# Performance work log

Measured on AMD Instinct MI355X. Metric: run time of the kernel, lower is better.

## Reference

```python
import jax, jax.numpy as jnp
import numpy as np

ALPHA = 0.34          # Ewald splitting parameter (init kwarg alpha)
MAX_HKL = 12          # init kwarg max_hkl
TWO_PI = 2.0 * np.pi


def setup_inputs() -> dict:
    key = jax.random.key(0)
    k1, k2 = jax.random.split(key)
    N = 4096
    L = 40.0  # cubic box edge (Angstrom)
    coords = jax.random.uniform(k1, (N, 3), dtype=jnp.float32) * L
    q = jax.random.normal(k2, (N,), dtype=jnp.float32)
    q = q - jnp.mean(q)  # neutral cell (k=0 term is excluded)
    box = jnp.eye(3, dtype=jnp.float32) * L
    return {"coords": coords, "box": box, "q": q}


def _ewald_recip_energy(coords, box, q):
    """Reciprocal-space Ewald sum over |h|,|k|,|l| <= MAX_HKL (rank=0 PME fallback).

    pot_i = (4*pi/V) * sum_{k!=0} exp(-|k|^2/(4 a^2))/|k|^2 * Re[S(k) exp(-i k.r_i)]
    E     = 0.5 * sum_i q_i * pot_i
    """
    K = MAX_HKL
    vol = jnp.abs(jnp.linalg.det(box))
    recip = TWO_PI * jnp.linalg.inv(box).T  # rows = reciprocal lattice vectors (3,3)
    h = jnp.arange(-K, K + 1)
    hh, kk, ll = jnp.meshgrid(h, h, h, indexing="ij")
    hkl = jnp.stack([hh.ravel(), kk.ravel(), ll.ravel()], axis=-1).astype(jnp.float32)  # (Nk,3)
    kvecs = hkl @ recip                      # (Nk,3)
    k2 = jnp.sum(kvecs * kvecs, axis=-1)     # (Nk,)
    nonzero = k2 > 0.0                       # mask out k = 0 (static shape, jit-safe)
    k2_safe = jnp.where(nonzero, k2, 1.0)
    inv_4a2 = 1.0 / (4.0 * ALPHA * ALPHA)
    fac = jnp.where(nonzero, jnp.exp(-k2_safe * inv_4a2) / k2_safe, 0.0)  # (Nk,)
    phases = coords @ kvecs.T                # (N, Nk)
    c = jnp.cos(phases)
    s = jnp.sin(phases)
    Sre = q @ c                              # (Nk,) Re S(k)
    Sim = q @ s                              # (Nk,) Im S(k)
    pref = (4.0 * np.pi) / vol
    # Re[S(k) e^{-i k.r_i}] = Sre*cos + Sim*sin
    pot = pref * (c @ (fac * Sre) + s @ (fac * Sim))  # (N,)
    return 0.5 * jnp.sum(q * pot)


def reference(coords, box, q):
    return _ewald_recip_energy(coords, box, q)
```

## Files before the change

### kernel.cpp

```cpp
#include <hip/hip_runtime.h>
#include <math.h>

namespace {
constexpr int   KMAX   = 12;
constexpr int   NLINE  = 313;
constexpr int   NGROUP = NLINE * 5;
constexpr int   NKV    = NGROUP * 5;
constexpr int   NSLICE = 8;
constexpr int   S2_BLOCKS = (NKV + 255) / 256;
constexpr float ALPHA_  = 0.34f;
constexpr float TWO_PI_ = 6.283185307179586f;
}

__device__ __forceinline__ void cofactors(const float* __restrict__ box,
                                          float C[3][3], float* det) {
  const float b00 = box[0], b01 = box[1], b02 = box[2];
  const float b10 = box[3], b11 = box[4], b12 = box[5];
  const float b20 = box[6], b21 = box[7], b22 = box[8];
  C[0][0] =  (b11 * b22 - b12 * b21);
  C[0][1] = -(b10 * b22 - b12 * b20);
  C[0][2] =  (b10 * b21 - b11 * b20);
  C[1][0] = -(b01 * b22 - b02 * b21);
  C[1][1] =  (b00 * b22 - b02 * b20);
  C[1][2] = -(b00 * b21 - b01 * b20);
  C[2][0] =  (b01 * b12 - b02 * b11);
  C[2][1] = -(b00 * b12 - b02 * b10);
  C[2][2] =  (b00 * b11 - b01 * b10);
  *det = b00 * C[0][0] + b01 * C[0][1] + b02 * C[0][2];
}

__device__ __forceinline__ void line_hk(int L, int* h, int* k) {
  if (L < 300)      { *h = L / 25 + 1; *k = L % 25 - 12; }
  else if (L < 312) { *h = 0;          *k = L - 299;     }
  else              { *h = 0;          *k = 0;           }
}

__global__ __launch_bounds__(256) void make_frac(
    const float* __restrict__ coords, const float* __restrict__ box,
    const float* __restrict__ q, int N, float4* __restrict__ frac,
    float* __restrict__ out)
{
  const int i = blockIdx.x * 256 + threadIdx.x;
  if (i == 0) out[0] = 0.0f;
  if (i >= N) return;
  float C[3][3], det;
  cofactors(box, C, &det);
  const float invdet = 1.0f / det;
  const float x = coords[3 * i + 0];
  const float y = coords[3 * i + 1];
  const float z = coords[3 * i + 2];
  float4 f;
  f.x = (x * C[0][0] + y * C[0][1] + z * C[0][2]) * invdet;
  f.y = (x * C[1][0] + y * C[1][1] + z * C[1][2]) * invdet;
  float c = (x * C[2][0] + y * C[2][1] + z * C[2][2]) * invdet;
  f.z = c - floorf(c);
  f.w = q[i];
  frac[i] = f;
}

__global__ __launch_bounds__(256, 8) void ewald_g5(
    const float4* __restrict__ frac, int N, float* __restrict__ partial)
{
  const int lane = threadIdx.x & 63;
  const int g    = blockIdx.x * 4 + (threadIdx.x >> 6);
  const int gc   = (g < NGROUP) ? g : (NGROUP - 1);

  int h, k; line_hk(gc / 5, &h, &k);
  const float hf  = (float)h;
  const float kf  = (float)k;
  const float l0f = (float)(-KMAX + 5 * (gc % 5));

  const int slice = blockIdx.y;
  const int sp    = (N + NSLICE - 1) / NSLICE;
  const int s_beg = slice * sp;
  const int s_end = min(s_beg + sp, N);

  float Sre[5] = {0.f, 0.f, 0.f, 0.f, 0.f};
  float Sim[5] = {0.f, 0.f, 0.f, 0.f, 0.f};

  for (int i = s_beg + lane; i < s_end; i += 64) {
    const float4 p = frac[i];
    float t = fmaf(hf, p.x, fmaf(kf, p.y, l0f * p.z));
    float tf;
    asm("v_fract_f32 %0, %1" : "=v"(tf) : "v"(t));
    float s0, c0, sr, cr;
    asm("v_sin_f32 %0, %1" : "=v"(s0) : "v"(tf));
    asm("v_cos_f32 %0, %1" : "=v"(c0) : "v"(tf));
    asm("v_sin_f32 %0, %1" : "=v"(sr) : "v"(p.z));
    asm("v_cos_f32 %0, %1" : "=v"(cr) : "v"(p.z));
    float Pre = p.w * c0, Pim = p.w * s0;
    Sre[0] += Pre; Sim[0] += Pim;
#pragma unroll
    for (int u = 1; u < 5; ++u) {
      const float nre = fmaf(Pre, cr, -(Pim * sr));
      const float nim = fmaf(Pre, sr,  (Pim * cr));
      Pre = nre; Pim = nim;
      Sre[u] += Pre; Sim[u] += Pim;
    }
  }

#pragma unroll
  for (int off = 32; off > 0; off >>= 1) {
#pragma unroll
    for (int u = 0; u < 5; ++u) {
      Sre[u] += __shfl_down(Sre[u], off);
      Sim[u] += __shfl_down(Sim[u], off);
    }
  }
  if (g < NGROUP && lane == 0) {
    float* dst = partial + (size_t)(g * NSLICE + slice) * 10;
#pragma unroll
    for (int u = 0; u < 5; ++u) {
      dst[2 * u + 0] = Sre[u];
      dst[2 * u + 1] = Sim[u];
    }
  }
}

__global__ __launch_bounds__(256) void stage2(
    const float* __restrict__ partial, const float* __restrict__ box,
    float* __restrict__ out)
{
  __shared__ float red[256];
  const int idx = blockIdx.x * 256 + threadIdx.x;
  float e = 0.f;
  if (idx < NKV) {
    const int g = idx / 5, u = idx % 5;
    const int L = g / 5, sub = g % 5;
    int h, k; line_hk(L, &h, &k);
    const int l = -KMAX + 5 * sub + u;
    if (!(h == 0 && k == 0 && l <= 0)) {
      float re = 0.f, im = 0.f;
      for (int s = 0; s < NSLICE; ++s) {
        const float* p = partial + (size_t)(g * NSLICE + s) * 10 + 2 * u;
        re += p[0]; im += p[1];
      }
      float C[3][3], det;
      cofactors(box, C, &det);
      const float invdet = 1.0f / det;
      const float hf = (float)h, kf = (float)k, lf = (float)l;
      const float kx = (hf * C[0][0] + kf * C[1][0] + lf * C[2][0]) * invdet;
      const float ky = (hf * C[0][1] + kf * C[1][1] + lf * C[2][1]) * invdet;
      const float kz = (hf * C[0][2] + kf * C[1][2] + lf * C[2][2]) * invdet;
      const float k2 = TWO_PI_ * TWO_PI_ * (kx * kx + ky * ky + kz * kz);
      const float fac = __expf(-k2 / (4.0f * ALPHA_ * ALPHA_)) / k2;
      e = fac * fmaf(re, re, im * im);
    }
  }
  red[threadIdx.x] = e;
  __syncthreads();
  for (int s = 128; s > 0; s >>= 1) {
    if (threadIdx.x < s) red[threadIdx.x] += red[threadIdx.x + s];
    __syncthreads();
  }
  if (threadIdx.x == 0) {
    float C[3][3], det;
    cofactors(box, C, &det);
    const float scale = (4.0f * 3.14159265358979323846f) / fabsf(det);
    atomicAdd(out, scale * red[0]);
  }
}

extern "C" void kernel_launch(void* const* d_in, const int* in_sizes, int n_in,
                              void* d_out, int out_size, void* d_ws, size_t ws_size,
                              hipStream_t stream) {
  const float* coords = (const float*)d_in[0];
  const float* box    = (const float*)d_in[1];
  const float* q      = (const float*)d_in[2];
  float* out = (float*)d_out;
  const int N = in_sizes[2];

  float4* frac    = (float4*)d_ws;
  float*  partial = (float*)((char*)d_ws + (128 << 10));

  hipLaunchKernelGGL(make_frac, dim3((N + 255) / 256), dim3(256), 0, stream,
                     coords, box, q, N, frac, out);
  const dim3 grid((NGROUP + 3) / 4, NSLICE);
  hipLaunchKernelGGL(ewald_g5, grid, dim3(256), 0, stream, frac, N, partial);
  hipLaunchKernelGGL(stage2, dim3(S2_BLOCKS), dim3(256), 0, stream,
                     partial, box, out);
}
```

Before: 24.96 us.

## Factor structure factors into hk-line by l GEMM on fp16 MFMA

Splits exp(i(h a + k b + l c)) into an (h,k) phase table and an l phase table, built as fp16 matrices over atoms. The per-k-vector sum then becomes a complex GEMM run with 16x16x32 fp16 MFMA instructions, and the per-atom sin/cos and complex rotation loops go away. The cost is writing about 5.7 MB of fp16 intermediates to workspace, plus reduced precision from fp16 operands. It also hardcodes KDIM=4096, which ties the kernel to N<=4096.

```diff
diff --git a/kernel.cpp b/kernel.cpp
--- a/kernel.cpp
+++ b/kernel.cpp
@@ -4,12 +4,20 @@
 namespace {
 constexpr int   KMAX   = 12;
 constexpr int   NLINE  = 313;
-constexpr int   NGROUP = NLINE * 5;
-constexpr int   NKV    = NGROUP * 5;
-constexpr int   NSLICE = 8;
+constexpr int   NL25   = 25;
+constexpr int   NKV    = NLINE * NL25;
+constexpr int   KDIM   = 4096;
+constexpr int   MROWS  = 640;
+constexpr int   NCOLS  = 64;
+constexpr int   NKS    = 8;
+constexpr int   KCHUNK = KDIM / NKS;
 constexpr int   S2_BLOCKS = (NKV + 255) / 256;
 constexpr float ALPHA_  = 0.34f;
 constexpr float TWO_PI_ = 6.283185307179586f;
+
+typedef __attribute__((ext_vector_type(4))) short    short4v;
+typedef __attribute__((ext_vector_type(8))) _Float16 half8;
+typedef __attribute__((ext_vector_type(4))) float    f32x4;
 }
 
 __device__ __forceinline__ void cofactors(const float* __restrict__ box,
@@ -35,105 +43,116 @@
   else              { *h = 0;          *k = 0;           }
 }
 
-__global__ __launch_bounds__(256) void make_frac(
+__global__ __launch_bounds__(256) void build_ab(
     const float* __restrict__ coords, const float* __restrict__ box,
-    const float* __restrict__ q, int N, float4* __restrict__ frac,
+    const float* __restrict__ q, int N,
+    _Float16* __restrict__ A2, _Float16* __restrict__ Bt,
     float* __restrict__ out)
 {
-  const int i = blockIdx.x * 256 + threadIdx.x;
-  if (i == 0) out[0] = 0.0f;
-  if (i >= N) return;
+  const int id = blockIdx.x * 256 + threadIdx.x;
+  if (id == 0) out[0] = 0.0f;
+
   float C[3][3], det;
   cofactors(box, C, &det);
   const float invdet = 1.0f / det;
-  const float x = coords[3 * i + 0];
-  const float y = coords[3 * i + 1];
-  const float z = coords[3 * i + 2];
-  float4 f;
-  f.x = (x * C[0][0] + y * C[0][1] + z * C[0][2]) * invdet;
-  f.y = (x * C[1][0] + y * C[1][1] + z * C[1][2]) * invdet;
-  float c = (x * C[2][0] + y * C[2][1] + z * C[2][2]) * invdet;
-  f.z = c - floorf(c);
-  f.w = q[i];
-  frac[i] = f;
-}
-
-__global__ __launch_bounds__(256, 8) void ewald_g5(
-    const float4* __restrict__ frac, int N, float* __restrict__ partial)
+
+  if (id < 320 * KDIM) {
+    const int Ls = id >> 12;
+    const int i  = id & (KDIM - 1);
+    float pr = 0.f, pi_ = 0.f;
+    if (Ls < NLINE && i < N) {
+      int h, k; line_hk(Ls, &h, &k);
+      const float x = coords[3 * i + 0];
+      const float y = coords[3 * i + 1];
+      const float z = coords[3 * i + 2];
+      const float a = (x * C[0][0] + y * C[0][1] + z * C[0][2]) * invdet;
+      const float b = (x * C[1][0] + y * C[1][1] + z * C[1][2]) * invdet;
+      float t = fmaf((float)h, a, (float)k * b);
+      float tf; asm("v_fract_f32 %0, %1" : "=v"(tf) : "v"(t));
+      float s0, c0;
+      asm("v_sin_f32 %0, %1" : "=v"(s0) : "v"(tf));
+      asm("v_cos_f32 %0, %1" : "=v"(c0) : "v"(tf));
+      const float qq = q[i];
+      pr = qq * c0; pi_ = qq * s0;
+    }
+    A2[(size_t)Ls * KDIM + i]         = (_Float16)pr;
+    A2[(size_t)(320 + Ls) * KDIM + i] = (_Float16)pi_;
+  } else {
+    const int j = id - 320 * KDIM;
+    if (j < 32 * KDIM) {
+      const int ls = j >> 12;
+      const int i  = j & (KDIM - 1);
+      float cr = 0.f, sr = 0.f;
+      if (ls < NL25 && i < N) {
+        const int l = ls - KMAX;
+        const float x = coords[3 * i + 0];
+        const float y = coords[3 * i + 1];
+        const float z = coords[3 * i + 2];
+        const float c = (x * C[2][0] + y * C[2][1] + z * C[2][2]) * invdet;
+        float t = (float)l * c;
+        float tf; asm("v_fract_f32 %0, %1" : "=v"(tf) : "v"(t));
+        asm("v_sin_f32 %0, %1" : "=v"(sr) : "v"(tf));
+        asm("v_cos_f32 %0, %1" : "=v"(cr) : "v"(tf));
+      }
+      Bt[(size_t)ls * KDIM + i]        = (_Float16)cr;
+      Bt[(size_t)(32 + ls) * KDIM + i] = (_Float16)sr;
+    }
+  }
+}
+
+__global__ __launch_bounds__(256) void gemm_sf(
+    const _Float16* __restrict__ A2, const _Float16* __restrict__ Bt,
+    float* __restrict__ Cp)
 {
+  const int w    = (blockIdx.x * 256 + threadIdx.x) >> 6;
   const int lane = threadIdx.x & 63;
-  const int g    = blockIdx.x * 4 + (threadIdx.x >> 6);
-  const int gc   = (g < NGROUP) ? g : (NGROUP - 1);
-
-  int h, k; line_hk(gc / 5, &h, &k);
-  const float hf  = (float)h;
-  const float kf  = (float)k;
-  const float l0f = (float)(-KMAX + 5 * (gc % 5));
-
-  const int slice = blockIdx.y;
-  const int sp    = (N + NSLICE - 1) / NSLICE;
-  const int s_beg = slice * sp;
-  const int s_end = min(s_beg + sp, N);
-
-  float Sre[5] = {0.f, 0.f, 0.f, 0.f, 0.f};
-  float Sim[5] = {0.f, 0.f, 0.f, 0.f, 0.f};
-
-  for (int i = s_beg + lane; i < s_end; i += 64) {
-    const float4 p = frac[i];
-    float t = fmaf(hf, p.x, fmaf(kf, p.y, l0f * p.z));
-    float tf;
-    asm("v_fract_f32 %0, %1" : "=v"(tf) : "v"(t));
-    float s0, c0, sr, cr;
-    asm("v_sin_f32 %0, %1" : "=v"(s0) : "v"(tf));
-    asm("v_cos_f32 %0, %1" : "=v"(c0) : "v"(tf));
-    asm("v_sin_f32 %0, %1" : "=v"(sr) : "v"(p.z));
-    asm("v_cos_f32 %0, %1" : "=v"(cr) : "v"(p.z));
-    float Pre = p.w * c0, Pim = p.w * s0;
-    Sre[0] += Pre; Sim[0] += Pim;
+  const int ks   = w & 7;
+  const int tile = w >> 3;
+  const int mt   = tile >> 2;
+  const int nt   = tile & 3;
+  const int r = lane & 15, g = lane >> 4;
+
+  const _Float16* arow = A2 + (size_t)(mt * 16 + r) * KDIM + ks * KCHUNK + g * 4;
+  const _Float16* brow = Bt + (size_t)(nt * 16 + r) * KDIM + ks * KCHUNK + g * 4;
+
+  f32x4 acc = {0.f, 0.f, 0.f, 0.f};
 #pragma unroll
-    for (int u = 1; u < 5; ++u) {
-      const float nre = fmaf(Pre, cr, -(Pim * sr));
-      const float nim = fmaf(Pre, sr,  (Pim * cr));
-      Pre = nre; Pim = nim;
-      Sre[u] += Pre; Sim[u] += Pim;
-    }
-  }
-
+  for (int st = 0; st < KCHUNK / 32; ++st) {
+    union { short4v s[2]; half8 h8; } ua, ub;
+    ua.s[0] = *(const short4v*)(arow + st * 32);
+    ua.s[1] = *(const short4v*)(arow + st * 32 + 16);
+    ub.s[0] = *(const short4v*)(brow + st * 32);
+    ub.s[1] = *(const short4v*)(brow + st * 32 + 16);
+    acc = __builtin_amdgcn_mfma_f32_16x16x32_f16(ua.h8, ub.h8, acc, 0, 0, 0);
+  }
+
+  float* ctile = Cp + ((size_t)ks * MROWS + mt * 16 + g * 4) * NCOLS + nt * 16 + r;
 #pragma unroll
-  for (int off = 32; off > 0; off >>= 1) {
-#pragma unroll
-    for (int u = 0; u < 5; ++u) {
-      Sre[u] += __shfl_down(Sre[u], off);
-      Sim[u] += __shfl_down(Sim[u], off);
-    }
-  }
-  if (g < NGROUP && lane == 0) {
-    float* dst = partial + (size_t)(g * NSLICE + slice) * 10;
-#pragma unroll
-    for (int u = 0; u < 5; ++u) {
-      dst[2 * u + 0] = Sre[u];
-      dst[2 * u + 1] = Sim[u];
-    }
-  }
+  for (int j = 0; j < 4; ++j) ctile[(size_t)j * NCOLS] = acc[j];
 }
 
 __global__ __launch_bounds__(256) void stage2(
-    const float* __restrict__ partial, const float* __restrict__ box,
+    const float* __restrict__ Cp, const float* __restrict__ box,
     float* __restrict__ out)
 {
   __shared__ float red[256];
   const int idx = blockIdx.x * 256 + threadIdx.x;
   float e = 0.f;
   if (idx < NKV) {
-    const int g = idx / 5, u = idx % 5;
-    const int L = g / 5, sub = g % 5;
+    const int L  = idx / NL25;
+    const int ls = idx % NL25;
+    const int l  = ls - KMAX;
     int h, k; line_hk(L, &h, &k);
-    const int l = -KMAX + 5 * sub + u;
     if (!(h == 0 && k == 0 && l <= 0)) {
-      float re = 0.f, im = 0.f;
-      for (int s = 0; s < NSLICE; ++s) {
-        const float* p = partial + (size_t)(g * NSLICE + s) * 10 + 2 * u;
-        re += p[0]; im += p[1];
+      float Sre = 0.f, Sim = 0.f;
+      for (int s = 0; s < NKS; ++s) {
+        const float* c0 = Cp + (size_t)s * MROWS * NCOLS;
+        const float prr = c0[(size_t)L * NCOLS + ls];
+        const float pri = c0[(size_t)L * NCOLS + 32 + ls];
+        const float pir = c0[(size_t)(320 + L) * NCOLS + ls];
+        const float pii = c0[(size_t)(320 + L) * NCOLS + 32 + ls];
+        Sre += prr - pii;
+        Sim += pri + pir;
       }
       float C[3][3], det;
       cofactors(box, C, &det);
@@ -144,7 +163,7 @@
       const float kz = (hf * C[0][2] + kf * C[1][2] + lf * C[2][2]) * invdet;
       const float k2 = TWO_PI_ * TWO_PI_ * (kx * kx + ky * ky + kz * kz);
       const float fac = __expf(-k2 / (4.0f * ALPHA_ * ALPHA_)) / k2;
-      e = fac * fmaf(re, re, im * im);
+      e = fac * fmaf(Sre, Sre, Sim * Sim);
     }
   }
   red[threadIdx.x] = e;
@@ -170,13 +189,14 @@
   float* out = (float*)d_out;
   const int N = in_sizes[2];
 
-  float4* frac    = (float4*)d_ws;
-  float*  partial = (float*)((char*)d_ws + (128 << 10));
-
-  hipLaunchKernelGGL(make_frac, dim3((N + 255) / 256), dim3(256), 0, stream,
-                     coords, box, q, N, frac, out);
-  const dim3 grid((NGROUP + 3) / 4, NSLICE);
-  hipLaunchKernelGGL(ewald_g5, grid, dim3(256), 0, stream, frac, N, partial);
+  _Float16* A2 = (_Float16*)d_ws;
+  _Float16* Bt = (_Float16*)((char*)d_ws + 5242880);
+  float*    Cp = (float*)   ((char*)d_ws + 5767168);
+
+  const int build_blocks = (352 * KDIM) / 256;
+  hipLaunchKernelGGL(build_ab, dim3(build_blocks), dim3(256), 0, stream,
+                     coords, box, q, N, A2, Bt, out);
+  hipLaunchKernelGGL(gemm_sf, dim3(320), dim3(256), 0, stream, A2, Bt, Cp);
   hipLaunchKernelGGL(stage2, dim3(S2_BLOCKS), dim3(256), 0, stream,
-                     partial, box, out);
-}
+                     Cp, box, out);
+}
```

Measured after the change: 32.79 us. 1.31x slower.
